# Optimization experiments

Hardware: AMD Instinct MI355X
Metric: run time of the kernel (lower is better)

The kernel has to match this reference:

```python
import jax, jax.numpy as jnp
import numpy as np

NUM_CLUSTERS = 64
DIM = 128
ALPHA = 100.0


def setup_inputs() -> dict:
    key = jax.random.key(0)
    k1, k2 = jax.random.split(key)
    x = jax.random.normal(k1, (32, 4096, DIM), dtype=jnp.float32)
    centroids = jax.random.uniform(k2, (NUM_CLUSTERS, DIM), dtype=jnp.float32)
    return {"x": x, "centroids": centroids}


def reference(x, centroids):
    # x: [B, N, D], centroids: [K, D]
    # Euclidean distances (torch.cdist p=2): [B, N, K]
    x2 = jnp.sum(x * x, axis=-1, keepdims=True)            # [B, N, 1]
    c2 = jnp.sum(centroids * centroids, axis=-1)            # [K]
    xc = jnp.einsum('bnd,kd->bnk', x, centroids)            # [B, N, K]
    dist2 = jnp.maximum(x2 + c2[None, None, :] - 2.0 * xc, 0.0)
    distances = jnp.sqrt(dist2)
    soft_assign = jax.nn.softmax(-ALPHA * distances, axis=2)  # [B, N, K]
    # vlad[b,k,:] = sum_n a[b,n,k] * (x[b,n,:] - c[k,:])
    vlad = jnp.einsum('bnk,bnd->bkd', soft_assign, x) \
         - jnp.sum(soft_assign, axis=1)[:, :, None] * centroids[None, :, :]
    B = x.shape[0]
    vlad = vlad.reshape(B, -1)
    # F.normalize(p=2, dim=1) with default eps=1e-12
    norm = jnp.maximum(jnp.linalg.norm(vlad, axis=1, keepdims=True), 1e-12)
    return vlad / norm
```

## Files before the change

kernel.cpp:

```cpp
#include <hip/hip_runtime.h>

typedef _Float16 half8 __attribute__((ext_vector_type(8)));
typedef _Float16 half4 __attribute__((ext_vector_type(4)));
typedef float floatx4 __attribute__((ext_vector_type(4)));

static constexpr int NB  = 32;
static constexpr int NP  = 4096;
static constexpr int DD  = 128;
static constexpr int KC  = 64;
static constexpr int TN  = 64;
static constexpr int TPB = 2;
static constexpr int SLOTS = NP / (TPB * TN);
static constexpr int STP = 72;

#define ALPHA_  100.0f
#define LOG2E_  1.44269504088896f

#define LGKM_BARRIER() asm volatile("s_waitcnt lgkmcnt(0)\ns_barrier" ::: "memory")

__global__ __launch_bounds__(256, 3)
void vlad_main(const float* __restrict__ xg, const float* __restrict__ cg,
               _Float16* __restrict__ vp, float* __restrict__ cpart)
{
    __shared__ __align__(16) _Float16 sxt[DD][STP];
    __shared__ __align__(16) _Float16 sat[KC][STP];
    __shared__ __align__(16) _Float16 schi[KC][DD];
    __shared__ float sc2[KC];

    const int tid  = threadIdx.x;
    const int lane = tid & 63;
    const int w    = tid >> 6;
    const int l15  = lane & 15;
    const int quad = lane >> 4;
    const int cswz = l15 & 7;
    const int b    = blockIdx.y;
    const int s    = blockIdx.x;
    const float* xb = xg + (size_t)b * NP * DD;

    const int nloc = w*16 + l15;
    const int scol = nloc ^ (quad << 4);
    const float* xpt = xb + (size_t)(s*TPB*TN + nloc)*DD + quad*8;

    float4 fa[4], fb[4];
#pragma unroll
    for (int ks = 0; ks < 4; ++ks) {
        fa[ks] = *(const float4*)(xpt + ks*32);
        fb[ks] = *(const float4*)(xpt + ks*32 + 4);
    }

    if (w == 0) {
#pragma unroll
        for (int mt = 0; mt < 4; ++mt) {
            float c2p = 0.f;
#pragma unroll
            for (int ks = 0; ks < 4; ++ks) {
                const float* p = cg + (mt*16 + l15)*DD + ks*32 + quad*8;
                float4 a  = *(const float4*)p;
                float4 bb = *(const float4*)(p + 4);
                half8 h;
                h[0]=(_Float16)a.x;  h[1]=(_Float16)a.y;  h[2]=(_Float16)a.z;  h[3]=(_Float16)a.w;
                h[4]=(_Float16)bb.x; h[5]=(_Float16)bb.y; h[6]=(_Float16)bb.z; h[7]=(_Float16)bb.w;
                *(half8*)&schi[mt*16 + l15][((ks*4 + quad) ^ cswz) * 8] = h;
                c2p += a.x*a.x + a.y*a.y + a.z*a.z + a.w*a.w
                     + bb.x*bb.x + bb.y*bb.y + bb.z*bb.z + bb.w*bb.w;
            }
            c2p += __shfl_xor(c2p, 16);
            c2p += __shfl_xor(c2p, 32);
            if (quad == 0) sc2[mt*16 + l15] = c2p;
        }
    }
    LGKM_BARRIER();

    floatx4 acc2[8];
#pragma unroll
    for (int i = 0; i < 8; ++i) acc2[i] = (floatx4){0.f, 0.f, 0.f, 0.f};
    floatx4 accs = (floatx4){0.f, 0.f, 0.f, 0.f};

    half8 onesf;
#pragma unroll
    for (int j = 0; j < 8; ++j) onesf[j] = (_Float16)((l15 == 0) ? 1.0f : 0.0f);

#pragma unroll
    for (int tt = 0; tt < TPB; ++tt) {
        half8 xf[4];
        float ssq = 0.f;
#pragma unroll
        for (int ks = 0; ks < 4; ++ks) {
            half8 h;
            h[0]=(_Float16)fa[ks].x; h[1]=(_Float16)fa[ks].y;
            h[2]=(_Float16)fa[ks].z; h[3]=(_Float16)fa[ks].w;
            h[4]=(_Float16)fb[ks].x; h[5]=(_Float16)fb[ks].y;
            h[6]=(_Float16)fb[ks].z; h[7]=(_Float16)fb[ks].w;
            xf[ks] = h;
            ssq += fa[ks].x*fa[ks].x + fa[ks].y*fa[ks].y + fa[ks].z*fa[ks].z + fa[ks].w*fa[ks].w
                 + fb[ks].x*fb[ks].x + fb[ks].y*fb[ks].y + fb[ks].z*fb[ks].z + fb[ks].w*fb[ks].w;
        }

        if (tt + 1 < TPB) {
            const float* xr = xpt + (size_t)(tt + 1) * TN * DD;
#pragma unroll
            for (int ks = 0; ks < 4; ++ks) {
                fa[ks] = *(const float4*)(xr + ks*32);
                fb[ks] = *(const float4*)(xr + ks*32 + 4);
            }
        }

        if (tt) LGKM_BARRIER();

#pragma unroll
        for (int ks = 0; ks < 4; ++ks)
#pragma unroll
            for (int j = 0; j < 8; ++j)
                sxt[ks*32 + quad*8 + j][scol] = xf[ks][j];

        floatx4 acc1[4];
#pragma unroll
        for (int mt = 0; mt < 4; ++mt) acc1[mt] = (floatx4){0.f, 0.f, 0.f, 0.f};
#pragma unroll
        for (int ks = 0; ks < 4; ++ks)
#pragma unroll
            for (int mt = 0; mt < 4; ++mt) {
                half8 cf = *(const half8*)&schi[mt*16 + l15][((ks*4 + quad) ^ cswz) * 8];
                acc1[mt] = __builtin_amdgcn_mfma_f32_16x16x32_f16(cf, xf[ks], acc1[mt], 0, 0, 0);
            }
        ssq += __shfl_xor(ssq, 16);
        ssq += __shfl_xor(ssq, 32);

        float dist[4][4];
#pragma unroll
        for (int mt = 0; mt < 4; ++mt) {
            floatx4 c2v = *(const floatx4*)&sc2[mt*16 + quad*4];
#pragma unroll
            for (int r = 0; r < 4; ++r) {
                float d2 = ssq + c2v[r] - 2.f*acc1[mt][r];
                dist[mt][r] = sqrtf(fmaxf(d2, 0.f));
            }
        }
        float dmin = dist[0][0];
#pragma unroll
        for (int mt = 0; mt < 4; ++mt)
#pragma unroll
            for (int r = 0; r < 4; ++r) dmin = fminf(dmin, dist[mt][r]);
        dmin = fminf(dmin, __shfl_xor(dmin, 16));
        dmin = fminf(dmin, __shfl_xor(dmin, 32));
        float pv[4][4];
        float psum = 0.f;
#pragma unroll
        for (int mt = 0; mt < 4; ++mt)
#pragma unroll
            for (int r = 0; r < 4; ++r) {
                float e = exp2f((dmin - dist[mt][r]) * (ALPHA_ * LOG2E_));
                pv[mt][r] = e; psum += e;
            }
        psum += __shfl_xor(psum, 16);
        psum += __shfl_xor(psum, 32);
        float invs = 1.0f / psum;
#pragma unroll
        for (int mt = 0; mt < 4; ++mt)
#pragma unroll
            for (int r = 0; r < 4; ++r)
                sat[mt*16 + quad*4 + r][scol] = (_Float16)(pv[mt][r] * invs);

        LGKM_BARRIER();

#pragma unroll
        for (int ks2 = 0; ks2 < 2; ++ks2) {
            const int nbase = ks2*32 + quad*8;
            half8 af = *(const half8*)&sat[w*16 + l15][nbase ^ ((l15 >> 2) << 4)];
            accs = __builtin_amdgcn_mfma_f32_16x16x32_f16(af, onesf, accs, 0, 0, 0);
#pragma unroll
            for (int nt = 0; nt < 8; ++nt) {
                const int d = nt*16 + l15;
                half8 bf = *(const half8*)&sxt[d][nbase ^ (((d >> 3) & 3) << 4)];
                acc2[nt] = __builtin_amdgcn_mfma_f32_16x16x32_f16(af, bf, acc2[nt], 0, 0, 0);
            }
        }
    }

    _Float16* slot = vp + ((size_t)b*SLOTS + s) * (KC*DD);
#pragma unroll
    for (int nt = 0; nt < 8; ++nt)
#pragma unroll
        for (int r = 0; r < 4; ++r) {
            int k = w*16 + quad*4 + r;
            int d = nt*16 + l15;
            __builtin_nontemporal_store((_Float16)acc2[nt][r], &slot[k*DD + d]);
        }
    if (l15 == 0) {
#pragma unroll
        for (int r = 0; r < 4; ++r)
            __builtin_nontemporal_store(accs[r],
                &cpart[((size_t)b*SLOTS + s)*KC + w*16 + quad*4 + r]);
    }
}

__global__ __launch_bounds__(256)
void vlad_reduce(const _Float16* __restrict__ vp, const float* __restrict__ cpart,
                 const float* __restrict__ cg, float* __restrict__ vfull,
                 float* __restrict__ ssp)
{
    __shared__ float scs[KC];
    __shared__ float red[4];
    const int b   = blockIdx.x >> 3;
    const int q   = blockIdx.x & 7;
    const int tid = threadIdx.x;

    if (tid < KC) {
        float cs = 0.f;
#pragma unroll
        for (int si = 0; si < SLOTS; ++si)
            cs += cpart[((size_t)b*SLOTS + si)*KC + tid];
        scs[tid] = cs;
    }
    __syncthreads();

    const int idx = q*1024 + tid*4;
    const _Float16* vpb = vp + (size_t)b*SLOTS*(KC*DD) + idx;
    floatx4 a = (floatx4){0.f, 0.f, 0.f, 0.f};
#pragma unroll
    for (int si = 0; si < SLOTS; ++si) {
        half4 t = __builtin_nontemporal_load((const half4*)(vpb + (size_t)si*(KC*DD)));
        a += __builtin_convertvector(t, floatx4);
    }
    float cs = scs[idx >> 7];
    floatx4 cv = *(const floatx4*)(cg + idx);
    a -= cs * cv;
    *(floatx4*)(vfull + (size_t)b*(KC*DD) + idx) = a;
    float ss = a[0]*a[0] + a[1]*a[1] + a[2]*a[2] + a[3]*a[3];
#pragma unroll
    for (int m = 1; m < 64; m <<= 1) ss += __shfl_xor(ss, m);
    if ((tid & 63) == 0) red[tid >> 6] = ss;
    __syncthreads();
    if (tid == 0) ssp[b*8 + q] = red[0] + red[1] + red[2] + red[3];
}

__global__ __launch_bounds__(256)
void vlad_norm(const float* __restrict__ vfull, const float* __restrict__ ssp,
               float* __restrict__ out)
{
    const int b   = blockIdx.x;
    const int tid = threadIdx.x;
    float tot = 0.f;
#pragma unroll
    for (int q = 0; q < 8; ++q) tot += ssp[b*8 + q];
    float scale = 1.0f / fmaxf(sqrtf(tot), 1e-12f);
#pragma unroll
    for (int i = 0; i < 8; ++i) {
        int idx = i*1024 + tid*4;
        floatx4 v = *(const floatx4*)(vfull + (size_t)b*(KC*DD) + idx);
        v *= scale;
        *(floatx4*)(out + (size_t)b*(KC*DD) + idx) = v;
    }
}

extern "C" void kernel_launch(void* const* d_in, const int* in_sizes, int n_in,
                              void* d_out, int out_size, void* d_ws, size_t ws_size,
                              hipStream_t stream)
{
    (void)in_sizes; (void)n_in; (void)out_size; (void)ws_size;
    const float* x = (const float*)d_in[0];
    const float* c = (const float*)d_in[1];
    float* out      = (float*)d_out;
    _Float16* vp    = (_Float16*)d_ws;
    float* cpart    = (float*)(vp + (size_t)NB*SLOTS*KC*DD);
    float* vfull    = cpart + (size_t)NB*SLOTS*KC;
    float* ssp      = vfull + (size_t)NB*KC*DD;

    vlad_main<<<dim3(SLOTS, NB), 256, 0, stream>>>(x, c, vp, cpart);
    vlad_reduce<<<NB*8, 256, 0, stream>>>(vp, cpart, c, vfull, ssp);
    vlad_norm<<<NB, 256, 0, stream>>>(vfull, ssp, out);
}
```

Before: 116.1 us.

## Balance tile work across a single wave of blocks and widen norm grid

```diff
diff --git a/kernel.cpp b/kernel.cpp
--- a/kernel.cpp
+++ b/kernel.cpp
@@ -9,8 +9,8 @@
 static constexpr int DD  = 128;
 static constexpr int KC  = 64;
 static constexpr int TN  = 64;
-static constexpr int TPB = 2;
-static constexpr int SLOTS = NP / (TPB * TN);
+static constexpr int BPB = 24;
+static constexpr int SLOTS = BPB;
 static constexpr int STP = 72;
 
 #define ALPHA_  100.0f
@@ -35,17 +35,19 @@
     const int cswz = l15 & 7;
     const int b    = blockIdx.y;
     const int s    = blockIdx.x;
+    const int t0   = (s < 16) ? s*3 : 48 + (s - 16)*2;
+    const int ntl  = (s < 16) ? 3 : 2;
     const float* xb = xg + (size_t)b * NP * DD;
 
     const int nloc = w*16 + l15;
     const int scol = nloc ^ (quad << 4);
-    const float* xpt = xb + (size_t)(s*TPB*TN + nloc)*DD + quad*8;
-
-    float4 fa[4], fb[4];
+    const float* xpt = xb + (size_t)(t0*TN + nloc)*DD + quad*8;
+
+    floatx4 fa[4], fb[4];
 #pragma unroll
     for (int ks = 0; ks < 4; ++ks) {
-        fa[ks] = *(const float4*)(xpt + ks*32);
-        fb[ks] = *(const float4*)(xpt + ks*32 + 4);
+        fa[ks] = __builtin_nontemporal_load((const floatx4*)(xpt + ks*32));
+        fb[ks] = __builtin_nontemporal_load((const floatx4*)(xpt + ks*32 + 4));
     }
 
     if (w == 0) {
@@ -55,14 +57,14 @@
 #pragma unroll
             for (int ks = 0; ks < 4; ++ks) {
                 const float* p = cg + (mt*16 + l15)*DD + ks*32 + quad*8;
-                float4 a  = *(const float4*)p;
-                float4 bb = *(const float4*)(p + 4);
+                floatx4 a  = *(const floatx4*)p;
+                floatx4 bb = *(const floatx4*)(p + 4);
                 half8 h;
-                h[0]=(_Float16)a.x;  h[1]=(_Float16)a.y;  h[2]=(_Float16)a.z;  h[3]=(_Float16)a.w;
-                h[4]=(_Float16)bb.x; h[5]=(_Float16)bb.y; h[6]=(_Float16)bb.z; h[7]=(_Float16)bb.w;
+                h[0]=(_Float16)a[0];  h[1]=(_Float16)a[1];  h[2]=(_Float16)a[2];  h[3]=(_Float16)a[3];
+                h[4]=(_Float16)bb[0]; h[5]=(_Float16)bb[1]; h[6]=(_Float16)bb[2]; h[7]=(_Float16)bb[3];
                 *(half8*)&schi[mt*16 + l15][((ks*4 + quad) ^ cswz) * 8] = h;
-                c2p += a.x*a.x + a.y*a.y + a.z*a.z + a.w*a.w
-                     + bb.x*bb.x + bb.y*bb.y + bb.z*bb.z + bb.w*bb.w;
+                c2p += a[0]*a[0] + a[1]*a[1] + a[2]*a[2] + a[3]*a[3]
+                     + bb[0]*bb[0] + bb[1]*bb[1] + bb[2]*bb[2] + bb[3]*bb[3];
             }
             c2p += __shfl_xor(c2p, 16);
             c2p += __shfl_xor(c2p, 32);
@@ -80,28 +82,27 @@
 #pragma unroll
     for (int j = 0; j < 8; ++j) onesf[j] = (_Float16)((l15 == 0) ? 1.0f : 0.0f);
 
-#pragma unroll
-    for (int tt = 0; tt < TPB; ++tt) {
+    for (int tt = 0; tt < ntl; ++tt) {
         half8 xf[4];
         float ssq = 0.f;
 #pragma unroll
         for (int ks = 0; ks < 4; ++ks) {
             half8 h;
-            h[0]=(_Float16)fa[ks].x; h[1]=(_Float16)fa[ks].y;
-            h[2]=(_Float16)fa[ks].z; h[3]=(_Float16)fa[ks].w;
-            h[4]=(_Float16)fb[ks].x; h[5]=(_Float16)fb[ks].y;
-            h[6]=(_Float16)fb[ks].z; h[7]=(_Float16)fb[ks].w;
+            h[0]=(_Float16)fa[ks][0]; h[1]=(_Float16)fa[ks][1];
+            h[2]=(_Float16)fa[ks][2]; h[3]=(_Float16)fa[ks][3];
+            h[4]=(_Float16)fb[ks][0]; h[5]=(_Float16)fb[ks][1];
+            h[6]=(_Float16)fb[ks][2]; h[7]=(_Float16)fb[ks][3];
             xf[ks] = h;
-            ssq += fa[ks].x*fa[ks].x + fa[ks].y*fa[ks].y + fa[ks].z*fa[ks].z + fa[ks].w*fa[ks].w
-                 + fb[ks].x*fb[ks].x + fb[ks].y*fb[ks].y + fb[ks].z*fb[ks].z + fb[ks].w*fb[ks].w;
-        }
-
-        if (tt + 1 < TPB) {
+            ssq += fa[ks][0]*fa[ks][0] + fa[ks][1]*fa[ks][1] + fa[ks][2]*fa[ks][2] + fa[ks][3]*fa[ks][3]
+                 + fb[ks][0]*fb[ks][0] + fb[ks][1]*fb[ks][1] + fb[ks][2]*fb[ks][2] + fb[ks][3]*fb[ks][3];
+        }
+
+        if (tt + 1 < ntl) {
             const float* xr = xpt + (size_t)(tt + 1) * TN * DD;
 #pragma unroll
             for (int ks = 0; ks < 4; ++ks) {
-                fa[ks] = *(const float4*)(xr + ks*32);
-                fb[ks] = *(const float4*)(xr + ks*32 + 4);
+                fa[ks] = __builtin_nontemporal_load((const floatx4*)(xr + ks*32));
+                fb[ks] = __builtin_nontemporal_load((const floatx4*)(xr + ks*32 + 4));
             }
         }
 
@@ -238,19 +239,17 @@
 void vlad_norm(const float* __restrict__ vfull, const float* __restrict__ ssp,
                float* __restrict__ out)
 {
-    const int b   = blockIdx.x;
+    const int b   = blockIdx.x >> 3;
+    const int q   = blockIdx.x & 7;
     const int tid = threadIdx.x;
     float tot = 0.f;
 #pragma unroll
-    for (int q = 0; q < 8; ++q) tot += ssp[b*8 + q];
+    for (int k = 0; k < 8; ++k) tot += ssp[b*8 + k];
     float scale = 1.0f / fmaxf(sqrtf(tot), 1e-12f);
-#pragma unroll
-    for (int i = 0; i < 8; ++i) {
-        int idx = i*1024 + tid*4;
-        floatx4 v = *(const floatx4*)(vfull + (size_t)b*(KC*DD) + idx);
-        v *= scale;
-        *(floatx4*)(out + (size_t)b*(KC*DD) + idx) = v;
-    }
+    const int idx = q*1024 + tid*4;
+    floatx4 v = *(const floatx4*)(vfull + (size_t)b*(KC*DD) + idx);
+    v *= scale;
+    *(floatx4*)(out + (size_t)b*(KC*DD) + idx) = v;
 }
 
 extern "C" void kernel_launch(void* const* d_in, const int* in_sizes, int n_in,
@@ -266,7 +265,7 @@
     float* vfull    = cpart + (size_t)NB*SLOTS*KC;
     float* ssp      = vfull + (size_t)NB*KC*DD;
 
-    vlad_main<<<dim3(SLOTS, NB), 256, 0, stream>>>(x, c, vp, cpart);
+    vlad_main<<<dim3(BPB, NB), 256, 0, stream>>>(x, c, vp, cpart);
     vlad_reduce<<<NB*8, 256, 0, stream>>>(vp, cpart, c, vfull, ssp);
-    vlad_norm<<<NB, 256, 0, stream>>>(vfull, ssp, out);
-}
+    vlad_norm<<<NB*8, 256, 0, stream>>>(vfull, ssp, out);
+}
```

New measurement: 122.7 us. +5.7%, slower.
